# Optimization experiments

Measured on AMD Instinct MI355X. Metric: run time of the kernel, lower is better.

Reference implementation:

```python
import jax, jax.numpy as jnp
import numpy as np

N_NODES = 100000
N_EDGES = 3200000
D_IN = 128
D_OUT = 128


def setup_inputs() -> dict:
    key = jax.random.key(0)
    kx, kw, kb, kr, kc, kv = jax.random.split(key, 6)
    x = jax.random.normal(kx, (N_NODES, D_IN), dtype=jnp.float32)
    W = jax.random.normal(kw, (D_OUT, D_IN), dtype=jnp.float32) * (1.0 / np.sqrt(D_IN))
    b = jax.random.normal(kb, (D_OUT,), dtype=jnp.float32) * 0.01
    adj_rows = jax.random.randint(kr, (N_EDGES,), 0, N_NODES, dtype=jnp.int32)
    adj_cols = jax.random.randint(kc, (N_EDGES,), 0, N_NODES, dtype=jnp.int32)
    adj_vals = jax.random.uniform(kv, (N_EDGES,), dtype=jnp.float32)
    return {"x": x, "W": W, "b": b, "adj_rows": adj_rows,
            "adj_cols": adj_cols, "adj_vals": adj_vals}


def reference(x, W, b, adj_rows, adj_cols, adj_vals):
    # linear: out = x @ W.T + b   -> [N, D_OUT]
    out = jnp.einsum('ni,oi->no', x, W) + b
    # spmm(adj, out): row r = sum over edges (r, c, v) of v * out[c]
    gathered = out[adj_cols] * adj_vals[:, None]          # [E, D_OUT]
    agg = jax.ops.segment_sum(gathered, adj_rows, num_segments=x.shape[0])
    return jax.nn.elu(agg)
```

## Files before the change

### kernel.cpp

```cpp
#include <hip/hip_runtime.h>
#include <hip/hip_bf16.h>
#include <cmath>

#define RPB      32
#define FB_CAP   1280
#define SB_SHIFT 11
#define NSB_MAX  64
#define TILE     2048
#define CH_PER_SB 34
#define CPAD     32

typedef __attribute__((ext_vector_type(8))) short short8;
typedef __attribute__((ext_vector_type(4))) float floatx4;

__device__ __forceinline__ unsigned short f2bf(float f) {
    unsigned int u = __float_as_uint(f);
    u += 0x7FFFu + ((u >> 16) & 1u);
    return (unsigned short)(u >> 16);
}

__global__ __launch_bounds__(256) void gemm_mfma_kernel(
    const float* __restrict__ x, const unsigned short* __restrict__ Wbg,
    const float* __restrict__ b, unsigned short* __restrict__ Yb, int N)
{
    __shared__ __align__(16) unsigned short Wb[128][136];
    __shared__ __align__(16) unsigned short Xb[64][136];
    const int t    = threadIdx.x;
    const int wave = t >> 6;
    const int lane = t & 63;
    const int col  = lane & 15;
    const int quad = lane >> 4;
    const int rowbase = blockIdx.x * 64;

#pragma unroll
    for (int i = 0; i < 8; ++i) {
        const int idx = t + 256 * i;
        const int o = idx >> 4, k8 = (idx & 15) * 8;
        *(uint4*)&Wb[o][k8] = *(const uint4*)&Wbg[idx * 8];
    }
#pragma unroll
    for (int i = 0; i < 8; ++i) {
        const int idx = t + 256 * i;
        const int row = idx >> 5, k4 = (idx & 31) * 4;
        const int gr = rowbase + row;
        float4 v = make_float4(0.f, 0.f, 0.f, 0.f);
        if (gr < N) v = *(const float4*)&x[(size_t)gr * 128 + k4];
        Xb[row][k4 + 0] = f2bf(v.x); Xb[row][k4 + 1] = f2bf(v.y);
        Xb[row][k4 + 2] = f2bf(v.z); Xb[row][k4 + 3] = f2bf(v.w);
    }
    __syncthreads();

    float bias[8];
#pragma unroll
    for (int nt = 0; nt < 8; ++nt) bias[nt] = b[nt * 16 + col];

    floatx4 acc[8] = {};
    const int mrow = wave * 16;
#pragma unroll
    for (int k0 = 0; k0 < 128; k0 += 32) {
        const short8 a = *(const short8*)&Xb[mrow + col][k0 + quad * 8];
#pragma unroll
        for (int nt = 0; nt < 8; ++nt) {
            const short8 bf = *(const short8*)&Wb[nt * 16 + col][k0 + quad * 8];
            acc[nt] = __builtin_amdgcn_mfma_f32_16x16x32_bf16(a, bf, acc[nt], 0, 0, 0);
        }
    }
#pragma unroll
    for (int nt = 0; nt < 8; ++nt) {
#pragma unroll
        for (int reg = 0; reg < 4; ++reg)
            Xb[mrow + quad * 4 + reg][nt * 16 + col] = f2bf(acc[nt][reg] + bias[nt]);
    }
    __syncthreads();
#pragma unroll
    for (int i = 0; i < 4; ++i) {
        const int idx = t + 256 * i;
        const int row = idx >> 4, c16 = (idx & 15) * 8;
        const int gr  = rowbase + row;
        if (gr < N)
            *(uint4*)&Yb[(size_t)gr * 128 + c16] = *(const uint4*)&Xb[row][c16];
    }
}

__global__ __launch_bounds__(256) void init_cursor_kernel(
    int* __restrict__ cursor1, int* __restrict__ cursor2, int SB_CAP, int NB,
    const float* __restrict__ W, unsigned short* __restrict__ Wbg)
{
    const int i = blockIdx.x * blockDim.x + threadIdx.x;
    if (i < NSB_MAX) cursor1[i * CPAD] = i * SB_CAP;
    if (i < NB)      cursor2[i] = i * FB_CAP;
    const int stride = gridDim.x * blockDim.x;
    for (int j = i; j < 128 * 128 / 4; j += stride) {
        const float4 v = ((const float4*)W)[j];
        uint2 u;
        u.x = (unsigned)f2bf(v.x) | ((unsigned)f2bf(v.y) << 16);
        u.y = (unsigned)f2bf(v.z) | ((unsigned)f2bf(v.w) << 16);
        ((uint2*)Wbg)[j] = u;
    }
}

__global__ __launch_bounds__(256) void pass1_kernel(
    const int* __restrict__ rows, const int* __restrict__ cols,
    const float* __restrict__ vals, int* __restrict__ cursor1,
    int2* __restrict__ pairs1, int E)
{
    __shared__ int2 sbuf[TILE];
    __shared__ unsigned char sbin[TILE];
    __shared__ unsigned short perm[TILE];
    __shared__ int hist[NSB_MAX], off[NSB_MAX], gbase[NSB_MAX], cur[NSB_MAX];
    const int t  = threadIdx.x;
    const int lane = t & 63;
    const int lo = blockIdx.x * TILE;
    const int cnt = min(TILE, E - lo);

    if (t < NSB_MAX) hist[t] = 0;
    __syncthreads();
    for (int i = t; i < cnt; i += 256) {
        const int   r = rows[lo + i];
        const int   c = cols[lo + i];
        const float v = vals[lo + i];
        sbuf[i] = make_int2(((r & 2047) << 17) | c, __float_as_int(v));
        const int bb = r >> SB_SHIFT;
        sbin[i] = (unsigned char)bb;
        atomicAdd(&hist[bb], 1);
    }
    __syncthreads();
    if (t < NSB_MAX) {
        const int h = hist[t];
        int s = h;
#pragma unroll
        for (int d = 1; d < NSB_MAX; d <<= 1) {
            const int n = __shfl_up(s, d);
            if (lane >= d) s += n;
        }
        off[t] = s - h;
        cur[t] = s - h;
        if (h > 0) gbase[t] = atomicAdd(&cursor1[t * CPAD], h);
    }
    __syncthreads();
    for (int i = t; i < cnt; i += 256) {
        const int pos = atomicAdd(&cur[sbin[i]], 1);
        perm[pos] = (unsigned short)i;
    }
    __syncthreads();
    for (int i = t; i < cnt; i += 256) {
        const int src = perm[i];
        const int bb  = sbin[src];
        pairs1[gbase[bb] + (i - off[bb])] = sbuf[src];
    }
}

__global__ __launch_bounds__(256) void pass2_kernel(
    const int* __restrict__ cursor1, int* __restrict__ cursor2,
    const int2* __restrict__ pairs1, int2* __restrict__ pairs2, int SB_CAP)
{
    __shared__ int2 sbuf[TILE];
    __shared__ unsigned short perm[TILE];
    __shared__ int hist[64], off[64], gbase[64], cur[64];
    const int t   = threadIdx.x;
    const int lane = t & 63;
    const int sb  = blockIdx.x / CH_PER_SB;
    const int ch  = blockIdx.x % CH_PER_SB;
    const int base = sb * SB_CAP;
    const int scnt = cursor1[sb * CPAD] - base;
    const int csz  = (scnt + CH_PER_SB - 1) / CH_PER_SB;
    const int lo   = ch * csz;
    const int cnt  = max(0, min(csz, scnt - lo));

    if (t < 64) hist[t] = 0;
    __syncthreads();
    for (int i = t; i < cnt; i += 256) {
        const int2 p = pairs1[base + lo + i];
        sbuf[i] = p;
        atomicAdd(&hist[(unsigned)p.x >> 22], 1);
    }
    __syncthreads();
    if (t < 64) {
        const int h = hist[t];
        int s = h;
#pragma unroll
        for (int d = 1; d < 64; d <<= 1) {
            const int n = __shfl_up(s, d);
            if (lane >= d) s += n;
        }
        off[t] = s - h;
        cur[t] = s - h;
        if (h > 0) gbase[t] = atomicAdd(&cursor2[sb * 64 + t], h);
    }
    __syncthreads();
    for (int i = t; i < cnt; i += 256) {
        const int pos = atomicAdd(&cur[(unsigned)sbuf[i].x >> 22], 1);
        perm[pos] = (unsigned short)i;
    }
    __syncthreads();
    for (int i = t; i < cnt; i += 256) {
        const int2 p = sbuf[perm[i]];
        const int bb = (unsigned)p.x >> 22;
        pairs2[gbase[bb] + (i - off[bb])] = make_int2(p.x & 0x3FFFFF, p.y);
    }
}

__global__ __launch_bounds__(256) void sortgather_kernel(
    const int* __restrict__ cursor2, const int2* __restrict__ pairs2,
    const unsigned int* __restrict__ Yu, float* __restrict__ out, int N)
{
    __shared__ __align__(16) int2 sbuf[FB_CAP];
    __shared__ __align__(16) int2 dbuf[FB_CAP + 4];
    __shared__ int hist[RPB];
    __shared__ int off[RPB];
    __shared__ int cur[RPB];
    __shared__ int rowtick;
    const int b    = blockIdx.x;
    const int t    = threadIdx.x;
    const int lane = t & 63;
    const int slot = b * FB_CAP;
    int cnt = cursor2[b] - slot;
    if (cnt > FB_CAP) cnt = FB_CAP;

    if (t < RPB) hist[t] = 0;
    if (t == 0) rowtick = 0;
    __syncthreads();
    for (int i = t; i < cnt; i += 256) {
        const int2 p = pairs2[slot + i];
        sbuf[i] = p;
        atomicAdd(&hist[p.x >> 17], 1);
    }
    __syncthreads();
    if (t == 0) {
        int run = 0;
#pragma unroll
        for (int k = 0; k < RPB; ++k) { off[k] = run; cur[k] = run; run += hist[k]; }
    }
    __syncthreads();
    for (int i = t; i < cnt; i += 256) {
        const int2 p   = sbuf[i];
        const int  pos = atomicAdd(&cur[p.x >> 17], 1);
        dbuf[pos] = make_int2(p.x & 0x1FFFF, p.y);
    }
    if (t < 4) dbuf[cnt + t] = make_int2(0, 0);
    __syncthreads();

    const int sub   = lane >> 4;
    const int qlane = lane & 15;

    for (;;) {
        int rl = 0;
        if (lane == 0) rl = atomicAdd(&rowtick, 1);
        rl = __shfl(rl, 0);
        if (rl >= RPB) break;
        const int gr = b * RPB + rl;
        if (gr >= N) continue;
        const int s = off[rl];
        const int e = s + hist[rl];

        float acc0 = 0.f, acc1 = 0.f, acc2 = 0.f, acc3 = 0.f;
        float acc4 = 0.f, acc5 = 0.f, acc6 = 0.f, acc7 = 0.f;
#pragma unroll 2
        for (int j = s; j < e; j += 4) {
            const int2 p = dbuf[j + sub];
            float v = __int_as_float(p.y);
            v = (j + sub < e) ? v : 0.0f;
            const uint4 y = *(const uint4*)&Yu[((unsigned)p.x << 6) + qlane * 4];
            acc0 = fmaf(v, __uint_as_float(y.x << 16), acc0);
            acc1 = fmaf(v, __uint_as_float(y.x & 0xFFFF0000u), acc1);
            acc2 = fmaf(v, __uint_as_float(y.y << 16), acc2);
            acc3 = fmaf(v, __uint_as_float(y.y & 0xFFFF0000u), acc3);
            acc4 = fmaf(v, __uint_as_float(y.z << 16), acc4);
            acc5 = fmaf(v, __uint_as_float(y.z & 0xFFFF0000u), acc5);
            acc6 = fmaf(v, __uint_as_float(y.w << 16), acc6);
            acc7 = fmaf(v, __uint_as_float(y.w & 0xFFFF0000u), acc7);
        }
        acc0 += __shfl_xor(acc0, 32); acc1 += __shfl_xor(acc1, 32);
        acc2 += __shfl_xor(acc2, 32); acc3 += __shfl_xor(acc3, 32);
        acc4 += __shfl_xor(acc4, 32); acc5 += __shfl_xor(acc5, 32);
        acc6 += __shfl_xor(acc6, 32); acc7 += __shfl_xor(acc7, 32);
        acc0 += __shfl_xor(acc0, 16); acc1 += __shfl_xor(acc1, 16);
        acc2 += __shfl_xor(acc2, 16); acc3 += __shfl_xor(acc3, 16);
        acc4 += __shfl_xor(acc4, 16); acc5 += __shfl_xor(acc5, 16);
        acc6 += __shfl_xor(acc6, 16); acc7 += __shfl_xor(acc7, 16);

        if (lane < 16) {
            float4 o0, o1;
            o0.x = acc0 > 0.f ? acc0 : __expf(acc0) - 1.f;
            o0.y = acc1 > 0.f ? acc1 : __expf(acc1) - 1.f;
            o0.z = acc2 > 0.f ? acc2 : __expf(acc2) - 1.f;
            o0.w = acc3 > 0.f ? acc3 : __expf(acc3) - 1.f;
            o1.x = acc4 > 0.f ? acc4 : __expf(acc4) - 1.f;
            o1.y = acc5 > 0.f ? acc5 : __expf(acc5) - 1.f;
            o1.z = acc6 > 0.f ? acc6 : __expf(acc6) - 1.f;
            o1.w = acc7 > 0.f ? acc7 : __expf(acc7) - 1.f;
            float* po = &out[(size_t)gr * 128 + qlane * 8];
            *(float4*)po       = o0;
            *(float4*)(po + 4) = o1;
        }
    }
}

__global__ __launch_bounds__(256) void gemm_bias_kernel(
    const float* __restrict__ x, const float* __restrict__ W,
    const float* __restrict__ b, float* __restrict__ Y, int N)
{
    __shared__ float Wt[128][130];
    const int tid  = threadIdx.x;
    const int wave = tid >> 6;
    const int lane = tid & 63;
    for (int i = tid; i < 128 * 128; i += 256) {
        const int o = i >> 7, k = i & 127;
        Wt[k][o] = W[i];
    }
    __syncthreads();
    const float2 bv = *(const float2*)&b[2 * lane];
    for (int row = blockIdx.x * 4 + wave; row < N; row += gridDim.x * 4) {
        float acc0 = 0.f, acc1 = 0.f;
        for (int k = 0; k < 128; ++k) {
            const float2 w = *(const float2*)&Wt[k][2 * lane];
            const float xv = x[(size_t)row * 128 + k];
            acc0 = fmaf(xv, w.x, acc0);
            acc1 = fmaf(xv, w.y, acc1);
        }
        float2 o2; o2.x = acc0 + bv.x; o2.y = acc1 + bv.y;
        *(float2*)&Y[(size_t)row * 128 + 2 * lane] = o2;
    }
}

__global__ __launch_bounds__(256) void scatter_kernel(
    const int* __restrict__ rows, const int* __restrict__ cols,
    const float* __restrict__ vals, const float* __restrict__ Y,
    float* __restrict__ out, int E)
{
    const long long gid = (long long)blockIdx.x * blockDim.x + threadIdx.x;
    const int wid  = (int)(gid >> 6);
    const int lane = threadIdx.x & 63;
    if (wid >= E) return;
    const int   r = rows[wid];
    const int   c = cols[wid];
    const float v = vals[wid];
    const float2 y = *(const float2*)&Y[(size_t)c * 128 + 2 * lane];
    float* po = &out[(size_t)r * 128 + 2 * lane];
    atomicAdd(po,     v * y.x);
    atomicAdd(po + 1, v * y.y);
}

__global__ __launch_bounds__(256) void elu_kernel(float* __restrict__ out, int n4)
{
    int i = blockIdx.x * blockDim.x + threadIdx.x;
    const int stride = gridDim.x * blockDim.x;
    float4* p = (float4*)out;
    for (; i < n4; i += stride) {
        float4 v = p[i];
        v.x = v.x > 0.f ? v.x : expf(v.x) - 1.f;
        v.y = v.y > 0.f ? v.y : expf(v.y) - 1.f;
        v.z = v.z > 0.f ? v.z : expf(v.z) - 1.f;
        v.w = v.w > 0.f ? v.w : expf(v.w) - 1.f;
        p[i] = v;
    }
}

extern "C" void kernel_launch(void* const* d_in, const int* in_sizes, int n_in,
                              void* d_out, int out_size, void* d_ws, size_t ws_size,
                              hipStream_t stream)
{
    const float* x    = (const float*)d_in[0];
    const float* W    = (const float*)d_in[1];
    const float* b    = (const float*)d_in[2];
    const int*   rows = (const int*)d_in[3];
    const int*   cols = (const int*)d_in[4];
    const float* vals = (const float*)d_in[5];
    float* out = (float*)d_out;

    const int N   = in_sizes[0] / 128;
    const int E   = in_sizes[3];
    const int NB  = (N + RPB - 1) / RPB;
    const int NSB = (N + (1 << SB_SHIFT) - 1) >> SB_SHIFT;

    const int sb_mean = (E + NSB - 1) / NSB;
    int sbsig = 1; while (sbsig * sbsig < sb_mean) ++sbsig;
    const int SB_CAP = (sb_mean + 10 * sbsig + 63) & ~63;

    auto align256 = [](size_t v) { return (v + 255) & ~(size_t)255; };
    const size_t offPairs2 = 0;
    const size_t szPairs2  = (size_t)NB * FB_CAP * 8;
    const size_t offShared = align256(offPairs2 + szPairs2);
    const size_t szShared  = (size_t)NSB * SB_CAP * 8 > (size_t)N * 256
                           ? (size_t)NSB * SB_CAP * 8 : (size_t)N * 256;
    const size_t offCur1   = align256(offShared + szShared);
    const size_t offCur2   = align256(offCur1 + (size_t)NSB_MAX * 4 * CPAD);
    const size_t offWb     = align256(offCur2 + (size_t)NB * 4);
    const size_t need      = offWb + 128 * 128 * 2;

    const bool csr_ok = (need <= ws_size) && (NSB <= NSB_MAX) &&
                        ((long long)E <= (long long)NB * 1056) &&
                        (SB_CAP <= CH_PER_SB * TILE);

    if (csr_ok) {
        int2* pairs2        = (int2*)((char*)d_ws + offPairs2);
        int2* pairs1        = (int2*)((char*)d_ws + offShared);
        unsigned short* Yb  = (unsigned short*)((char*)d_ws + offShared);
        int*  cursor1       = (int*)((char*)d_ws + offCur1);
        int*  cursor2       = (int*)((char*)d_ws + offCur2);
        unsigned short* Wbg = (unsigned short*)((char*)d_ws + offWb);

        init_cursor_kernel<<<(NB + 255) / 256, 256, 0, stream>>>(cursor1, cursor2,
                                                                 SB_CAP, NB, W, Wbg);
        pass1_kernel<<<(E + TILE - 1) / TILE, 256, 0, stream>>>(rows, cols, vals,
                                                                cursor1, pairs1, E);
        pass2_kernel<<<NSB * CH_PER_SB, 256, 0, stream>>>(cursor1, cursor2,
                                                          pairs1, pairs2, SB_CAP);
        gemm_mfma_kernel<<<(N + 63) / 64, 256, 0, stream>>>(x, Wbg, b, Yb, N);
        sortgather_kernel<<<NB, 256, 0, stream>>>(cursor2, pairs2,
                                                  (const unsigned int*)Yb, out, N);
    } else {
        float* Y = (float*)d_ws;
        hipMemsetAsync(d_out, 0, (size_t)out_size * sizeof(float), stream);
        gemm_bias_kernel<<<512, 256, 0, stream>>>(x, W, b, Y, N);
        scatter_kernel<<<(E + 3) / 4, 256, 0, stream>>>(rows, cols, vals, Y, out, E);
        elu_kernel<<<1024, 256, 0, stream>>>(out, out_size / 4);
    }
}
```

Baseline: 298.7 us.

## Fuse GEMM and edge-binning pass into one interleaved launch with separate buffers

```diff
diff --git a/kernel.cpp b/kernel.cpp
--- a/kernel.cpp
+++ b/kernel.cpp
@@ -19,24 +19,25 @@
     return (unsigned short)(u >> 16);
 }
 
-__global__ __launch_bounds__(256) void gemm_mfma_kernel(
-    const float* __restrict__ x, const unsigned short* __restrict__ Wbg,
-    const float* __restrict__ b, unsigned short* __restrict__ Yb, int N)
-{
-    __shared__ __align__(16) unsigned short Wb[128][136];
-    __shared__ __align__(16) unsigned short Xb[64][136];
+__device__ __forceinline__ void gemm_body(
+    char* smraw, const float* __restrict__ x,
+    const unsigned short* __restrict__ Wbg, const float* __restrict__ b,
+    unsigned short* __restrict__ Yb, int N, int blk)
+{
+    unsigned short* Wb = (unsigned short*)smraw;
+    unsigned short* Xb = Wb + 128 * 136;
     const int t    = threadIdx.x;
     const int wave = t >> 6;
     const int lane = t & 63;
     const int col  = lane & 15;
     const int quad = lane >> 4;
-    const int rowbase = blockIdx.x * 64;
+    const int rowbase = blk * 64;
 
 #pragma unroll
     for (int i = 0; i < 8; ++i) {
         const int idx = t + 256 * i;
         const int o = idx >> 4, k8 = (idx & 15) * 8;
-        *(uint4*)&Wb[o][k8] = *(const uint4*)&Wbg[idx * 8];
+        *(uint4*)&Wb[o * 136 + k8] = *(const uint4*)&Wbg[idx * 8];
     }
 #pragma unroll
     for (int i = 0; i < 8; ++i) {
@@ -45,8 +46,8 @@
         const int gr = rowbase + row;
         float4 v = make_float4(0.f, 0.f, 0.f, 0.f);
         if (gr < N) v = *(const float4*)&x[(size_t)gr * 128 + k4];
-        Xb[row][k4 + 0] = f2bf(v.x); Xb[row][k4 + 1] = f2bf(v.y);
-        Xb[row][k4 + 2] = f2bf(v.z); Xb[row][k4 + 3] = f2bf(v.w);
+        Xb[row * 136 + k4 + 0] = f2bf(v.x); Xb[row * 136 + k4 + 1] = f2bf(v.y);
+        Xb[row * 136 + k4 + 2] = f2bf(v.z); Xb[row * 136 + k4 + 3] = f2bf(v.w);
     }
     __syncthreads();
 
@@ -58,10 +59,10 @@
     const int mrow = wave * 16;
 #pragma unroll
     for (int k0 = 0; k0 < 128; k0 += 32) {
-        const short8 a = *(const short8*)&Xb[mrow + col][k0 + quad * 8];
+        const short8 a = *(const short8*)&Xb[(mrow + col) * 136 + k0 + quad * 8];
 #pragma unroll
         for (int nt = 0; nt < 8; ++nt) {
-            const short8 bf = *(const short8*)&Wb[nt * 16 + col][k0 + quad * 8];
+            const short8 bf = *(const short8*)&Wb[(nt * 16 + col) * 136 + k0 + quad * 8];
             acc[nt] = __builtin_amdgcn_mfma_f32_16x16x32_bf16(a, bf, acc[nt], 0, 0, 0);
         }
     }
@@ -69,7 +70,8 @@
     for (int nt = 0; nt < 8; ++nt) {
 #pragma unroll
         for (int reg = 0; reg < 4; ++reg)
-            Xb[mrow + quad * 4 + reg][nt * 16 + col] = f2bf(acc[nt][reg] + bias[nt]);
+            Xb[(mrow + quad * 4 + reg) * 136 + nt * 16 + col] =
+                f2bf(acc[nt][reg] + bias[nt]);
     }
     __syncthreads();
 #pragma unroll
@@ -78,8 +80,96 @@
         const int row = idx >> 4, c16 = (idx & 15) * 8;
         const int gr  = rowbase + row;
         if (gr < N)
-            *(uint4*)&Yb[(size_t)gr * 128 + c16] = *(const uint4*)&Xb[row][c16];
-    }
+            *(uint4*)&Yb[(size_t)gr * 128 + c16] = *(const uint4*)&Xb[row * 136 + c16];
+    }
+}
+
+__device__ __forceinline__ void pass1_body(
+    char* smraw, const int* __restrict__ rows, const int* __restrict__ cols,
+    const float* __restrict__ vals, int* __restrict__ cursor1,
+    int2* __restrict__ pairs1, int E, int blk)
+{
+    int2* sbuf           = (int2*)smraw;
+    unsigned char* sbin  = (unsigned char*)(sbuf + TILE);
+    unsigned short* perm = (unsigned short*)(sbin + TILE);
+    int* hist  = (int*)(perm + TILE);
+    int* off   = hist + NSB_MAX;
+    int* gbase = off + NSB_MAX;
+    int* cur   = gbase + NSB_MAX;
+    const int t  = threadIdx.x;
+    const int lane = t & 63;
+    const int lo = blk * TILE;
+    const int cnt = min(TILE, E - lo);
+
+    if (t < NSB_MAX) hist[t] = 0;
+    __syncthreads();
+    for (int i = t; i < cnt; i += 256) {
+        const int   r = rows[lo + i];
+        const int   c = cols[lo + i];
+        const float v = vals[lo + i];
+        sbuf[i] = make_int2(((r & 2047) << 17) | c, __float_as_int(v));
+        const int bb = r >> SB_SHIFT;
+        sbin[i] = (unsigned char)bb;
+        atomicAdd(&hist[bb], 1);
+    }
+    __syncthreads();
+    if (t < NSB_MAX) {
+        const int h = hist[t];
+        int s = h;
+#pragma unroll
+        for (int d = 1; d < NSB_MAX; d <<= 1) {
+            const int n = __shfl_up(s, d);
+            if (lane >= d) s += n;
+        }
+        off[t] = s - h;
+        cur[t] = s - h;
+        if (h > 0) gbase[t] = atomicAdd(&cursor1[t * CPAD], h);
+    }
+    __syncthreads();
+    for (int i = t; i < cnt; i += 256) {
+        const int pos = atomicAdd(&cur[sbin[i]], 1);
+        perm[pos] = (unsigned short)i;
+    }
+    __syncthreads();
+    for (int i = t; i < cnt; i += 256) {
+        const int src = perm[i];
+        const int bb  = sbin[src];
+        pairs1[gbase[bb] + (i - off[bb])] = sbuf[src];
+    }
+}
+
+__global__ __launch_bounds__(256) void fused_gemm_pass1_kernel(
+    const float* __restrict__ x, const unsigned short* __restrict__ Wbg,
+    const float* __restrict__ b, unsigned short* __restrict__ Yb, int N, int GB,
+    const int* __restrict__ rows, const int* __restrict__ cols,
+    const float* __restrict__ vals, int* __restrict__ cursor1,
+    int2* __restrict__ pairs1, int E, int PB)
+{
+    extern __shared__ __align__(16) char smraw[];
+    const int bid = blockIdx.x;
+    const int mn  = min(GB, PB);
+    int type, sub;
+    if (bid < 2 * mn) { type = bid & 1; sub = bid >> 1; }
+    else              { type = (GB > PB) ? 0 : 1; sub = mn + (bid - 2 * mn); }
+    if (type == 0) gemm_body(smraw, x, Wbg, b, Yb, N, sub);
+    else           pass1_body(smraw, rows, cols, vals, cursor1, pairs1, E, sub);
+}
+
+__global__ __launch_bounds__(256) void gemm_mfma_kernel(
+    const float* __restrict__ x, const unsigned short* __restrict__ Wbg,
+    const float* __restrict__ b, unsigned short* __restrict__ Yb, int N)
+{
+    __shared__ __align__(16) char sm[(128 * 136 + 64 * 136) * 2];
+    gemm_body(sm, x, Wbg, b, Yb, N, blockIdx.x);
+}
+
+__global__ __launch_bounds__(256) void pass1_kernel(
+    const int* __restrict__ rows, const int* __restrict__ cols,
+    const float* __restrict__ vals, int* __restrict__ cursor1,
+    int2* __restrict__ pairs1, int E)
+{
+    __shared__ __align__(16) char sm[TILE * 8 + TILE + TILE * 2 + NSB_MAX * 16];
+    pass1_body(sm, rows, cols, vals, cursor1, pairs1, E, blockIdx.x);
 }
 
 __global__ __launch_bounds__(256) void init_cursor_kernel(
@@ -96,57 +186,6 @@
         u.x = (unsigned)f2bf(v.x) | ((unsigned)f2bf(v.y) << 16);
         u.y = (unsigned)f2bf(v.z) | ((unsigned)f2bf(v.w) << 16);
         ((uint2*)Wbg)[j] = u;
-    }
-}
-
-__global__ __launch_bounds__(256) void pass1_kernel(
-    const int* __restrict__ rows, const int* __restrict__ cols,
-    const float* __restrict__ vals, int* __restrict__ cursor1,
-    int2* __restrict__ pairs1, int E)
-{
-    __shared__ int2 sbuf[TILE];
-    __shared__ unsigned char sbin[TILE];
-    __shared__ unsigned short perm[TILE];
-    __shared__ int hist[NSB_MAX], off[NSB_MAX], gbase[NSB_MAX], cur[NSB_MAX];
-    const int t  = threadIdx.x;
-    const int lane = t & 63;
-    const int lo = blockIdx.x * TILE;
-    const int cnt = min(TILE, E - lo);
-
-    if (t < NSB_MAX) hist[t] = 0;
-    __syncthreads();
-    for (int i = t; i < cnt; i += 256) {
-        const int   r = rows[lo + i];
-        const int   c = cols[lo + i];
-        const float v = vals[lo + i];
-        sbuf[i] = make_int2(((r & 2047) << 17) | c, __float_as_int(v));
-        const int bb = r >> SB_SHIFT;
-        sbin[i] = (unsigned char)bb;
-        atomicAdd(&hist[bb], 1);
-    }
-    __syncthreads();
-    if (t < NSB_MAX) {
-        const int h = hist[t];
-        int s = h;
-#pragma unroll
-        for (int d = 1; d < NSB_MAX; d <<= 1) {
-            const int n = __shfl_up(s, d);
-            if (lane >= d) s += n;
-        }
-        off[t] = s - h;
-        cur[t] = s - h;
-        if (h > 0) gbase[t] = atomicAdd(&cursor1[t * CPAD], h);
-    }
-    __syncthreads();
-    for (int i = t; i < cnt; i += 256) {
-        const int pos = atomicAdd(&cur[sbin[i]], 1);
-        perm[pos] = (unsigned short)i;
-    }
-    __syncthreads();
-    for (int i = t; i < cnt; i += 256) {
-        const int src = perm[i];
-        const int bb  = sbin[src];
-        pairs1[gbase[bb] + (i - off[bb])] = sbuf[src];
     }
 }
 
@@ -381,24 +420,52 @@
     const size_t offPairs2 = 0;
     const size_t szPairs2  = (size_t)NB * FB_CAP * 8;
     const size_t offShared = align256(offPairs2 + szPairs2);
-    const size_t szShared  = (size_t)NSB * SB_CAP * 8 > (size_t)N * 256
-                           ? (size_t)NSB * SB_CAP * 8 : (size_t)N * 256;
-    const size_t offCur1   = align256(offShared + szShared);
-    const size_t offCur2   = align256(offCur1 + (size_t)NSB_MAX * 4 * CPAD);
-    const size_t offWb     = align256(offCur2 + (size_t)NB * 4);
-    const size_t need      = offWb + 128 * 128 * 2;
+    const size_t szPairs1  = (size_t)NSB * SB_CAP * 8;
+    const size_t szY       = (size_t)N * 256;
+    const size_t szShared  = szPairs1 > szY ? szPairs1 : szY;
+    const size_t offCur1_a = align256(offShared + szShared);
+    const size_t offCur2_a = align256(offCur1_a + (size_t)NSB_MAX * 4 * CPAD);
+    const size_t offWb_a   = align256(offCur2_a + (size_t)NB * 4);
+    const size_t need      = offWb_a + 128 * 128 * 2;
+    const size_t offPairs1 = offShared;
+    const size_t offY      = align256(offPairs1 + szPairs1);
+    const size_t offCur1_o = align256(offY + szY);
+    const size_t offCur2_o = align256(offCur1_o + (size_t)NSB_MAX * 4 * CPAD);
+    const size_t offWb_o   = align256(offCur2_o + (size_t)NB * 4);
+    const size_t need_ovl  = offWb_o + 128 * 128 * 2;
 
     const bool csr_ok = (need <= ws_size) && (NSB <= NSB_MAX) &&
                         ((long long)E <= (long long)NB * 1056) &&
                         (SB_CAP <= CH_PER_SB * TILE);
-
-    if (csr_ok) {
+    const bool ovl_ok = csr_ok && (need_ovl <= ws_size);
+
+    if (ovl_ok) {
+        int2* pairs2        = (int2*)((char*)d_ws + offPairs2);
+        int2* pairs1        = (int2*)((char*)d_ws + offPairs1);
+        unsigned short* Yb  = (unsigned short*)((char*)d_ws + offY);
+        int*  cursor1       = (int*)((char*)d_ws + offCur1_o);
+        int*  cursor2       = (int*)((char*)d_ws + offCur2_o);
+        unsigned short* Wbg = (unsigned short*)((char*)d_ws + offWb_o);
+
+        const int GB = (N + 63) / 64;
+        const int PB = (E + TILE - 1) / TILE;
+        const int smsz = (128 * 136 + 64 * 136) * 2;
+
+        init_cursor_kernel<<<(NB + 255) / 256, 256, 0, stream>>>(cursor1, cursor2,
+                                                                 SB_CAP, NB, W, Wbg);
+        fused_gemm_pass1_kernel<<<GB + PB, 256, smsz, stream>>>(
+            x, Wbg, b, Yb, N, GB, rows, cols, vals, cursor1, pairs1, E, PB);
+        pass2_kernel<<<NSB * CH_PER_SB, 256, 0, stream>>>(cursor1, cursor2,
+                                                          pairs1, pairs2, SB_CAP);
+        sortgather_kernel<<<NB, 256, 0, stream>>>(cursor2, pairs2,
+                                                  (const unsigned int*)Yb, out, N);
+    } else if (csr_ok) {
         int2* pairs2        = (int2*)((char*)d_ws + offPairs2);
         int2* pairs1        = (int2*)((char*)d_ws + offShared);
         unsigned short* Yb  = (unsigned short*)((char*)d_ws + offShared);
-        int*  cursor1       = (int*)((char*)d_ws + offCur1);
-        int*  cursor2       = (int*)((char*)d_ws + offCur2);
-        unsigned short* Wbg = (unsigned short*)((char*)d_ws + offWb);
+        int*  cursor1       = (int*)((char*)d_ws + offCur1_a);
+        int*  cursor2       = (int*)((char*)d_ws + offCur2_a);
+        unsigned short* Wbg = (unsigned short*)((char*)d_ws + offWb_a);
 
         init_cursor_kernel<<<(NB + 255) / 256, 256, 0, stream>>>(cursor1, cursor2,
                                                                  SB_CAP, NB, W, Wbg);
```

After: 283.2 us. -5.2%, faster.
